# Kernel optimization log

Measured on AMD Instinct MI355X. Metric: run time of the kernel, lower is better.

Reference implementation:

```python
import jax, jax.numpy as jnp
import numpy as np

B = 1
DEPTH = 2
DIM = 256
HEADS = 8
MLP = 1024
NUM_CLASS = 4
PATCHES = 512
N = PATCHES * (NUM_CLASS + 1)  # 2560
HD = DIM // HEADS


def setup_inputs() -> dict:
    key = jax.random.key(0)
    ks = jax.random.split(key, 8)
    s = lambda k, shape: jax.random.normal(k, shape, jnp.float32) * 0.02
    return {
        "x": jax.random.normal(ks[0], (B, N, DIM), jnp.float32),
        "mask": jax.random.randint(ks[1], (B, NUM_CLASS), 0, 2, jnp.int32),
        "ln1_g": jnp.ones((DEPTH, DIM), jnp.float32),
        "ln1_b": jnp.zeros((DEPTH, DIM), jnp.float32),
        "Wqkv": s(ks[2], (DEPTH, DIM, 3 * DIM)),  # qkv_bias=False
        "Wproj": s(ks[3], (DEPTH, DIM, DIM)),
        "bproj": jnp.zeros((DEPTH, DIM), jnp.float32),
        "ln2_g": jnp.ones((DEPTH, DIM), jnp.float32),
        "ln2_b": jnp.zeros((DEPTH, DIM), jnp.float32),
        "W1": s(ks[4], (DEPTH, DIM, MLP)),
        "b1": jnp.zeros((DEPTH, MLP), jnp.float32),
        "W2": s(ks[5], (DEPTH, MLP, DIM)),
        "b2": jnp.zeros((DEPTH, DIM), jnp.float32),
    }


def layer_norm(x, g, b, eps=1e-5):
    mu = jnp.mean(x, axis=-1, keepdims=True)
    var = jnp.var(x, axis=-1, keepdims=True)
    return (x - mu) * jax.lax.rsqrt(var + eps) * g + b


def build_mask(mask):
    # Vectorized equivalent of mask_gen_fusion: block-diagonal per modality,
    # fusion rows attend everything except columns of missing modalities.
    blk = jnp.arange(N) // PATCHES  # [N], values in 0..NUM_CLASS
    base = blk[:, None] == blk[None, :]  # block diagonal (incl. fusion block)
    fusion_row = blk == NUM_CLASS  # [N]
    col_fusion = blk == NUM_CLASS  # [N]
    mod_ok = mask[:, jnp.clip(blk, 0, NUM_CLASS - 1)] == 1  # [B, N]
    allowed = jnp.where(fusion_row[None, :, None],
                        col_fusion[None, None, :] | mod_ok[:, None, :],
                        base[None, :, :])
    return allowed  # [B, N, N] bool


def reference(x, mask, ln1_g, ln1_b, Wqkv, Wproj, bproj, ln2_g, ln2_b, W1, b1, W2, b2):
    allowed = build_mask(mask)  # [B, N, N]
    scale = HD ** -0.5
    attns = []
    for d in range(DEPTH):
        # MaskedResidual(MaskedPreNormDrop(MaskedAttention))
        h = layer_norm(x, ln1_g[d], ln1_b[d])
        qkv = (h @ Wqkv[d]).reshape(B, N, 3, HEADS, HD)
        q, k, v = jnp.transpose(qkv, (2, 0, 3, 1, 4))  # each [B, H, N, HD]
        scores = jnp.einsum('bhnd,bhmd->bhnm', q, k) * scale
        scores = jnp.where(allowed[:, None, :, :], scores, -jnp.inf)
        attn = jax.nn.softmax(scores, axis=-1)  # [B, H, N, N]
        o = jnp.einsum('bhnm,bhmd->bhnd', attn, v)
        o = jnp.transpose(o, (0, 2, 1, 3)).reshape(B, N, DIM)
        o = o @ Wproj[d] + bproj[d]
        x = x + o
        attns.append(attn)
        # Residual(PreNorm(FeedForward)); F.gelu is exact erf gelu
        h2 = layer_norm(x, ln2_g[d], ln2_b[d])
        ff = jax.nn.gelu(h2 @ W1[d] + b1[d], approximate=False) @ W2[d] + b2[d]
        x = x + ff
    return x, jnp.stack(attns)
```

## Files before the change

### kernel.cpp

```cpp
#include <hip/hip_runtime.h>

#define NTOK 2560
#define NN ((long)NTOK*NTOK)

typedef __attribute__((ext_vector_type(8))) short short8;
typedef __attribute__((ext_vector_type(4))) float f32x4;

__device__ __forceinline__ unsigned short f2bf(float f){
  union { float f; unsigned int u; } v; v.f = f;
  unsigned int u = v.u + 0x7fffu + ((v.u >> 16) & 1u);
  return (unsigned short)(u >> 16);
}

__device__ __forceinline__ f32x4 mfma16(short8 a, short8 b, f32x4 c){
  return __builtin_amdgcn_mfma_f32_16x16x32_bf16(a, b, c, 0, 0, 0);
}

__global__ __launch_bounds__(256) void wt_all_k(
    const float* __restrict__ Wqkv, const float* __restrict__ Wproj,
    const float* __restrict__ W1, const float* __restrict__ W2,
    unsigned short* __restrict__ wqkvt, unsigned short* __restrict__ wprojt,
    unsigned short* __restrict__ w1t, unsigned short* __restrict__ w2t)
{
  __shared__ unsigned short T[64][68];
  int j = blockIdx.x;
  int d = j >= 192; j -= d*192;
  const float* src; unsigned short* dst; int K, N, tk, tn;
  if (j < 48){        src = Wqkv  + d*196608; dst = wqkvt  + d*196608; K=256;  N=768;  tk=j/12; tn=j-tk*12; }
  else if (j < 64){   j-=48;  src = Wproj + d*65536;  dst = wprojt + d*65536;  K=256;  N=256;  tk=j>>2; tn=j&3; }
  else if (j < 128){  j-=64;  src = W1    + d*262144; dst = w1t    + d*262144; K=256;  N=1024; tk=j>>4; tn=j&15; }
  else {              j-=128; src = W2    + d*262144; dst = w2t    + d*262144; K=1024; N=256;  tk=j>>2; tn=j&3; }
  int k0 = tk*64, n0 = tn*64;
  int r = threadIdx.x >> 2, c0 = (threadIdx.x & 3) * 16;
  const float* p = src + (long)(k0+r)*N + n0 + c0;
  #pragma unroll
  for (int e4 = 0; e4 < 4; e4++){
    f32x4 v = *(const f32x4*)(p + e4*4);
    #pragma unroll
    for (int e = 0; e < 4; e++) T[r][c0 + e4*4 + e] = f2bf(v[e]);
  }
  __syncthreads();
  unsigned short* q = dst + (long)(n0+r)*K + k0 + c0;
  short8 o0, o1;
  #pragma unroll
  for (int e = 0; e < 8; e++){ o0[e] = (short)T[c0+e][r]; o1[e] = (short)T[c0+8+e][r]; }
  *(short8*)q = o0;
  *(short8*)(q+8) = o1;
}

__device__ __forceinline__ void p_unit_body(
    int u, const unsigned short* __restrict__ qbf, const unsigned short* __restrict__ kbf,
    const float* __restrict__ rinv_ws, float* __restrict__ attn_out,
    const int* __restrict__ mask, char* smem)
{
  float (*P32)[268] = (float (*)[268])smem;
  int tid = threadIdx.x, lane = tid & 63, w = tid >> 6;
  int cb = u % 5, t2 = u / 5, tile = t2 % 80, h = t2 / 80;
  int row0 = tile * 32;
  int rblk = row0 >> 9;
  unsigned bits;
  if (rblk < 4) bits = 1u << rblk;
  else {
    bits = 16u;
    #pragma unroll
    for (int m=0; m<4; m++) if (mask[m]==1) bits |= (1u<<m);
  }
  long base = (long)h*NN + (long)row0*NTOK + cb*512;
  if (!((bits >> cb) & 1)){
    f32x4 z = {0.f,0.f,0.f,0.f};
    #pragma unroll
    for (int i=0;i<16;i++){
      int idx = tid + i*256;
      int rl = idx >> 7, c4 = (idx & 127) << 2;
      *(f32x4*)&attn_out[base + (long)rl*NTOK + c4] = z;
    }
    return;
  }
  int kk = (lane>>4)*8, l15 = lane & 15, rgrp = (lane>>4)*4;
  short8 aq0 = *(const short8*)&qbf[(h*NTOK + row0 + l15)*32 + kk];
  short8 aq1 = *(const short8*)&qbf[(h*NTOK + row0 + 16 + l15)*32 + kk];
  float rinv[8];
  #pragma unroll
  for (int r=0;r<4;r++){
    rinv[r]   = rinv_ws[h*NTOK + row0 + rgrp + r];
    rinv[4+r] = rinv_ws[h*NTOK + row0 + 16 + rgrp + r];
  }
  #pragma unroll
  for (int hf=0; hf<2; hf++){
    #pragma unroll
    for (int ct=0; ct<4; ct++){
      int cl = w*64 + ct*16 + l15;
      short8 bk = *(const short8*)&kbf[(h*NTOK + cb*512 + hf*256 + cl)*32 + kk];
      f32x4 s0 = {}; s0 = mfma16(aq0, bk, s0);
      f32x4 s1 = {}; s1 = mfma16(aq1, bk, s1);
      #pragma unroll
      for (int r=0;r<4;r++){
        P32[rgrp + r][cl]      = __expf(s0[r]) * rinv[r];
        P32[16 + rgrp + r][cl] = __expf(s1[r]) * rinv[4+r];
      }
    }
    __syncthreads();
    long hbase = base + hf*256;
    #pragma unroll
    for (int j=0;j<8;j++){
      int qi = j*256 + tid;
      int rl = qi >> 6, qc = (qi & 63)*4;
      *(f32x4*)&attn_out[hbase + (long)rl*NTOK + qc] = *(const f32x4*)&P32[rl][qc];
    }
    __syncthreads();
  }
}

template<int EPI, bool LN>
__global__ __launch_bounds__(256) void gemm2_k(
    const void* __restrict__ Ap,
    const float* __restrict__ lng, const float* __restrict__ lnb,
    const unsigned short* __restrict__ Bt,
    int N, int K,
    const float* __restrict__ bias,
    const float* __restrict__ xin,
    float* __restrict__ xout,
    unsigned short* __restrict__ obf,
    unsigned short* __restrict__ qbf,
    unsigned short* __restrict__ kbf,
    unsigned short* __restrict__ vtbf,
    int gx, int pbase,
    const unsigned short* __restrict__ p_qbf, const unsigned short* __restrict__ p_kbf,
    const float* __restrict__ p_rinv, float* __restrict__ p_attn,
    const int* __restrict__ maskp)
{
  __shared__ __align__(16) char smem[34816];
  if ((int)blockIdx.x >= gx){
    int u = pbase + ((int)blockIdx.x - gx) * (int)gridDim.y + (int)blockIdx.y;
    p_unit_body(u, p_qbf, p_kbf, p_rinv, p_attn, maskp, smem);
    return;
  }
  unsigned short (*As)[136] = (unsigned short (*)[136])smem;
  unsigned short (*Bs)[136] = (unsigned short (*)[136])(smem + 17408);
  int tid = threadIdx.x, lane = tid & 63, w = tid >> 6;
  int wr = w >> 1, wc = w & 1;
  int m0 = blockIdx.y * 64, n0 = blockIdx.x * 64;
  int row = tid >> 2, q4 = tid & 3;
  int l15 = lane & 15;
  f32x4 acc[2][2] = {};

  float mu, inv;
  if (LN){
    const float* xrow = (const float*)Ap + (m0+row)*256;
    float s = 0.f, s2 = 0.f;
    #pragma unroll
    for (int j=0;j<8;j++){
      const float* p = xrow + (j*4+q4)*8;
      f32x4 va = *(const f32x4*)p;
      f32x4 vb = *(const f32x4*)(p+4);
      #pragma unroll
      for (int e=0;e<4;e++){ s += va[e]+vb[e]; s2 += va[e]*va[e]+vb[e]*vb[e]; }
    }
    s  += __shfl_xor(s, 1);  s2 += __shfl_xor(s2, 1);
    s  += __shfl_xor(s, 2);  s2 += __shfl_xor(s2, 2);
    mu = s * (1.f/256.f);
    inv = rsqrtf(s2*(1.f/256.f) - mu*mu + 1e-5f);
  }

  for (int k0 = 0; k0 < K; k0 += 128){
    if (LN){
      const float* xrow = (const float*)Ap + (m0+row)*256;
      #pragma unroll
      for (int jj=0;jj<4;jj++){
        int cl = (jj*4+q4)*8;
        int cg = k0 + cl;
        f32x4 va = *(const f32x4*)(xrow + cg);
        f32x4 vb = *(const f32x4*)(xrow + cg + 4);
        f32x4 ga = *(const f32x4*)&lng[cg], gb = *(const f32x4*)&lng[cg+4];
        f32x4 ba = *(const f32x4*)&lnb[cg], bb = *(const f32x4*)&lnb[cg+4];
        short8 o;
        #pragma unroll
        for (int e=0;e<4;e++){
          o[e]   = (short)f2bf((va[e]-mu)*inv*ga[e] + ba[e]);
          o[4+e] = (short)f2bf((vb[e]-mu)*inv*gb[e] + bb[e]);
        }
        *(short8*)&As[row][cl] = o;
      }
    } else {
      const unsigned short* Arow = (const unsigned short*)Ap + (long)(m0+row)*K + k0;
      #pragma unroll
      for (int jj=0;jj<4;jj++){
        int cl = q4*32 + jj*8;
        *(short8*)&As[row][cl] = *(const short8*)&Arow[cl];
      }
    }
    {
      const unsigned short* Brow = Bt + (long)(n0+row)*K + k0;
      #pragma unroll
      for (int jj=0;jj<4;jj++){
        int cl = q4*32 + jj*8;
        *(short8*)&Bs[row][cl] = *(const short8*)&Brow[cl];
      }
    }
    __syncthreads();
    #pragma unroll
    for (int ks=0; ks<4; ks++){
      int kc = ks*32 + (lane>>4)*8;
      short8 a0 = *(const short8*)&As[wr*32 + l15][kc];
      short8 a1 = *(const short8*)&As[wr*32 + 16 + l15][kc];
      short8 b0 = *(const short8*)&Bs[wc*32 + l15][kc];
      short8 b1 = *(const short8*)&Bs[wc*32 + 16 + l15][kc];
      acc[0][0] = mfma16(a0,b0,acc[0][0]);
      acc[0][1] = mfma16(a0,b1,acc[0][1]);
      acc[1][0] = mfma16(a1,b0,acc[1][0]);
      acc[1][1] = mfma16(a1,b1,acc[1][1]);
    }
    if (k0 + 128 < K) __syncthreads();
  }

  #pragma unroll
  for (int rt=0; rt<2; rt++)
  #pragma unroll
  for (int ct=0; ct<2; ct++)
  #pragma unroll
  for (int r=0; r<4; r++){
    int rg = m0 + wr*32 + rt*16 + (lane>>4)*4 + r;
    int cg = n0 + wc*32 + ct*16 + l15;
    float v = acc[rt][ct][r];
    if (EPI == 0){
      int which = cg >> 8, h = (cg >> 5) & 7, hd = cg & 31;
      if (which == 0)      qbf[(h*NTOK + rg)*32 + hd] = f2bf(v * 0.17677669529663687f);
      else if (which == 1) kbf[(h*NTOK + rg)*32 + hd] = f2bf(v);
      else                 vtbf[(h*32 + hd)*NTOK + rg] = f2bf(v);
    } else if (EPI == 1){
      xout[rg*N + cg] = xin[rg*N + cg] + v + bias[cg];
    } else {
      float t = v + bias[cg];
      float ge = 0.5f * t * (1.f + erff(t * 0.70710678118654752f));
      obf[rg*N + cg] = f2bf(ge);
    }
  }
}

__global__ __launch_bounds__(256) void attn_o_k(
    const unsigned short* __restrict__ qbf,
    const unsigned short* __restrict__ kbf,
    const unsigned short* __restrict__ vtbf,
    const int* __restrict__ mask,
    float* __restrict__ rinv_ws,
    unsigned short* __restrict__ obf)
{
  __shared__ __align__(16) char asmem[34816];
  __shared__ float reds[4][32];
  __shared__ float rowinv_s[32];
  float (*P32)[268] = (float (*)[268])asmem;
  float (*O_red)[32][32] = (float (*)[32][32])asmem;

  int tid = threadIdx.x, lane = tid & 63, w = tid >> 6;
  int row0 = blockIdx.x * 32, h = blockIdx.y;
  int rblk = row0 >> 9;
  unsigned bits;
  if (rblk < 4) bits = 1u << rblk;
  else {
    bits = 16u;
    #pragma unroll
    for (int m=0; m<4; m++) if (mask[m] == 1) bits |= (1u << m);
  }
  int kk = (lane >> 4) * 8;
  int l15 = lane & 15;
  int rgrp = (lane >> 4) * 4;
  short8 aq0 = *(const short8*)&qbf[(h*NTOK + row0 + l15)*32 + kk];
  short8 aq1 = *(const short8*)&qbf[(h*NTOK + row0 + 16 + l15)*32 + kk];

  float s_[8] = {0,0,0,0,0,0,0,0};
  f32x4 oacc[2][2] = {};
  for (int b=0; b<5; b++){
    if (!((bits >> b) & 1)) continue;
    #pragma unroll
    for (int hf=0; hf<2; hf++){
      #pragma unroll
      for (int ct=0; ct<4; ct++){
        int cl = w*64 + ct*16 + l15;
        short8 bk = *(const short8*)&kbf[(h*NTOK + b*512 + hf*256 + cl)*32 + kk];
        f32x4 s0 = {}; s0 = mfma16(aq0, bk, s0);
        f32x4 s1 = {}; s1 = mfma16(aq1, bk, s1);
        #pragma unroll
        for (int r=0;r<4;r++){
          float e0 = __expf(s0[r]), e1 = __expf(s1[r]);
          s_[r] += e0; s_[4+r] += e1;
          P32[rgrp + r][cl] = e0;
          P32[16 + rgrp + r][cl] = e1;
        }
      }
      __syncthreads();
      #pragma unroll
      for (int ks2=0; ks2<2; ks2++){
        int kb = (w*2 + ks2)*32 + kk;
        f32x4 pa0a = *(const f32x4*)&P32[l15][kb],      pa0b = *(const f32x4*)&P32[l15][kb+4];
        f32x4 pa1a = *(const f32x4*)&P32[16 + l15][kb], pa1b = *(const f32x4*)&P32[16 + l15][kb+4];
        short8 pa0, pa1;
        #pragma unroll
        for (int e=0;e<4;e++){
          pa0[e] = (short)f2bf(pa0a[e]); pa0[4+e] = (short)f2bf(pa0b[e]);
          pa1[e] = (short)f2bf(pa1a[e]); pa1[4+e] = (short)f2bf(pa1b[e]);
        }
        #pragma unroll
        for (int hc=0; hc<2; hc++){
          short8 bv = *(const short8*)&vtbf[(h*32 + hc*16 + l15)*NTOK + b*512 + hf*256 + kb];
          oacc[0][hc] = mfma16(pa0, bv, oacc[0][hc]);
          oacc[1][hc] = mfma16(pa1, bv, oacc[1][hc]);
        }
      }
      __syncthreads();
    }
  }
  #pragma unroll
  for (int msk=1; msk<16; msk<<=1)
    #pragma unroll
    for (int i=0;i<8;i++) s_[i] += __shfl_xor(s_[i], msk);
  if (l15 == 0){
    #pragma unroll
    for (int r=0;r<4;r++){ reds[w][rgrp + r] = s_[r]; reds[w][16 + rgrp + r] = s_[4+r]; }
  }
  __syncthreads();
  if (tid < 32){
    float invv = 1.f / (reds[0][tid] + reds[1][tid] + reds[2][tid] + reds[3][tid]);
    rowinv_s[tid] = invv;
    rinv_ws[h*NTOK + row0 + tid] = invv;
  }
  __syncthreads();
  #pragma unroll
  for (int rt=0; rt<2; rt++)
    #pragma unroll
    for (int hc=0; hc<2; hc++)
      #pragma unroll
      for (int r=0; r<4; r++)
        O_red[w][rt*16 + rgrp + r][hc*16 + l15] = oacc[rt][hc][r];
  __syncthreads();
  #pragma unroll
  for (int i2=0; i2<2; i2++){
    int i = tid + i2*256;
    int rl = i >> 4, c2 = (i & 15) * 2;
    float invv = rowinv_s[rl];
    float o0 = (O_red[0][rl][c2]   + O_red[1][rl][c2]   + O_red[2][rl][c2]   + O_red[3][rl][c2]) * invv;
    float o1 = (O_red[0][rl][c2+1] + O_red[1][rl][c2+1] + O_red[2][rl][c2+1] + O_red[3][rl][c2+1]) * invv;
    unsigned int pk = (unsigned int)f2bf(o0) | ((unsigned int)f2bf(o1) << 16);
    *(unsigned int*)&obf[(row0 + rl)*256 + h*32 + c2] = pk;
  }
}

extern "C" void kernel_launch(void* const* d_in, const int* in_sizes, int n_in,
                              void* d_out, int out_size, void* d_ws, size_t ws_size,
                              hipStream_t stream)
{
  const float* x_in  = (const float*)d_in[0];
  const int*   maskp = (const int*)d_in[1];
  const float* ln1g  = (const float*)d_in[2];
  const float* ln1b  = (const float*)d_in[3];
  const float* Wqkv  = (const float*)d_in[4];
  const float* Wproj = (const float*)d_in[5];
  const float* bproj = (const float*)d_in[6];
  const float* ln2g  = (const float*)d_in[7];
  const float* ln2b  = (const float*)d_in[8];
  const float* W1    = (const float*)d_in[9];
  const float* b1    = (const float*)d_in[10];
  const float* W2    = (const float*)d_in[11];
  const float* b2    = (const float*)d_in[12];
  float* out = (float*)d_out;

  char* ws = (char*)d_ws;
  float* x              = (float*)(ws + 0);
  unsigned short* mbf   = (unsigned short*)(ws + 2621440);
  unsigned short* obf   = (unsigned short*)(ws + 7864320);
  unsigned short* qbf   = (unsigned short*)(ws + 9175040);
  unsigned short* kbf   = (unsigned short*)(ws + 10485760);
  unsigned short* vtbf  = (unsigned short*)(ws + 11796480);
  float* rinv           = (float*)(ws + 13107200);
  unsigned short* wqkvt = (unsigned short*)(ws + 13238272);
  unsigned short* wprojt= (unsigned short*)(ws + 14024704);
  unsigned short* w1t   = (unsigned short*)(ws + 14286848);
  unsigned short* w2t   = (unsigned short*)(ws + 15335424);

  wt_all_k<<<384, 256, 0, stream>>>(Wqkv, Wproj, W1, W2, wqkvt, wprojt, w1t, w2t);

  for (int d=0; d<2; d++){
    const float* xsrc = d ? x : x_in;
    float* attn = out + 655360 + (long)d*52428800;
    gemm2_k<0,true><<<dim3(12,40), 256, 0, stream>>>(xsrc, ln1g + d*256, ln1b + d*256,
        wqkvt + d*196608, 768, 256, nullptr, nullptr, nullptr, nullptr, qbf, kbf, vtbf,
        12, 0, nullptr, nullptr, nullptr, nullptr, nullptr);
    attn_o_k<<<dim3(80,8), 256, 0, stream>>>(qbf, kbf, vtbf, maskp, rinv, obf);
    gemm2_k<1,false><<<dim3(24,40), 256, 0, stream>>>(obf, nullptr, nullptr,
        wprojt + d*65536, 256, 256, bproj + d*256, xsrc, x, nullptr, nullptr, nullptr, nullptr,
        4, 0, qbf, kbf, rinv, attn, maskp);
    gemm2_k<2,true><<<dim3(46,40), 256, 0, stream>>>(x, ln2g + d*256, ln2b + d*256,
        w1t + d*262144, 1024, 256, b1 + d*1024, nullptr, nullptr, mbf, nullptr, nullptr, nullptr,
        16, 800, qbf, kbf, rinv, attn, maskp);
    float* xo = d ? out : x;
    gemm2_k<1,false><<<dim3(34,40), 256, 0, stream>>>(mbf, nullptr, nullptr,
        w2t + d*262144, 256, 1024, b2 + d*256, x, xo, nullptr, nullptr, nullptr, nullptr,
        4, 2000, qbf, kbf, rinv, attn, maskp);
  }
}
```

Baseline: 192.1 us.

## Fuse proj+LN2+MLP into one tail kernel and split attn zero-fill from P compute

Replaces the proj, FC1 and FC2 GEMM launches with a single tail kernel. Each 64-row block computes the projection plus residual, LayerNorm2, FC1 with GELU and FC2 on-chip, so the bf16 MLP intermediate never goes to global memory. The attention-probability output work is split into zero-fill units and real-compute units. Zero fills run alongside the QKV GEMM and the attention kernel, and the masked-in probability tiles are enumerated explicitly inside the tail kernel instead of being branch-tested per unit. This cuts launches and memory traffic, but the fused tail may have limited parallelism (40 row blocks) and heavier register use.

```diff
diff --git a/kernel.cpp b/kernel.cpp
--- a/kernel.cpp
+++ b/kernel.cpp
@@ -48,34 +48,46 @@
   *(short8*)(q+8) = o1;
 }
 
+__device__ __forceinline__ void zero_unit_body(int u, const int* __restrict__ mask,
+                                               float* __restrict__ attn_out)
+{
+  int h = u / 320, rem = u - h*320;
+  int tile, cb;
+  if (rem < 256){
+    tile = rem >> 2;
+    int zi = rem & 3, rblk = tile >> 4;
+    cb = zi + (zi >= rblk);
+  } else {
+    int fz = rem - 256;
+    tile = 64 + (fz >> 2);
+    cb = fz & 3;
+    if (mask[cb] == 1) return;
+  }
+  long base = (long)h*NN + (long)tile*32*NTOK + cb*512;
+  f32x4 z = {0.f,0.f,0.f,0.f};
+  int tid = threadIdx.x;
+  #pragma unroll
+  for (int i=0;i<16;i++){
+    int idx = tid + i*256;
+    int rl = idx >> 7, c4 = (idx & 127) << 2;
+    *(f32x4*)&attn_out[base + (long)rl*NTOK + c4] = z;
+  }
+}
+
 __device__ __forceinline__ void p_unit_body(
     int u, const unsigned short* __restrict__ qbf, const unsigned short* __restrict__ kbf,
     const float* __restrict__ rinv_ws, float* __restrict__ attn_out,
     const int* __restrict__ mask, char* smem)
 {
+  if (u >= 1152) return;
+  int h, tile, cb;
+  if (u < 512){ h = u >> 6; tile = u & 63; cb = tile >> 4; }
+  else if (u < 640){ int v = u - 512; h = v >> 4; tile = 64 + (v & 15); cb = 4; }
+  else { int v = u - 640; h = v >> 6; tile = 64 + ((v >> 2) & 15); cb = v & 3; if (mask[cb] != 1) return; }
   float (*P32)[268] = (float (*)[268])smem;
   int tid = threadIdx.x, lane = tid & 63, w = tid >> 6;
-  int cb = u % 5, t2 = u / 5, tile = t2 % 80, h = t2 / 80;
   int row0 = tile * 32;
-  int rblk = row0 >> 9;
-  unsigned bits;
-  if (rblk < 4) bits = 1u << rblk;
-  else {
-    bits = 16u;
-    #pragma unroll
-    for (int m=0; m<4; m++) if (mask[m]==1) bits |= (1u<<m);
-  }
   long base = (long)h*NN + (long)row0*NTOK + cb*512;
-  if (!((bits >> cb) & 1)){
-    f32x4 z = {0.f,0.f,0.f,0.f};
-    #pragma unroll
-    for (int i=0;i<16;i++){
-      int idx = tid + i*256;
-      int rl = idx >> 7, c4 = (idx & 127) << 2;
-      *(f32x4*)&attn_out[base + (long)rl*NTOK + c4] = z;
-    }
-    return;
-  }
   int kk = (lane>>4)*8, l15 = lane & 15, rgrp = (lane>>4)*4;
   short8 aq0 = *(const short8*)&qbf[(h*NTOK + row0 + l15)*32 + kk];
   short8 aq1 = *(const short8*)&qbf[(h*NTOK + row0 + 16 + l15)*32 + kk];
@@ -111,7 +123,7 @@
   }
 }
 
-template<int EPI, bool LN>
+template<int EPI, bool LN, int CG>
 __global__ __launch_bounds__(256) void gemm2_k(
     const void* __restrict__ Ap,
     const float* __restrict__ lng, const float* __restrict__ lnb,
@@ -124,15 +136,16 @@
     unsigned short* __restrict__ qbf,
     unsigned short* __restrict__ kbf,
     unsigned short* __restrict__ vtbf,
-    int gx, int pbase,
+    int gx, int zbase,
     const unsigned short* __restrict__ p_qbf, const unsigned short* __restrict__ p_kbf,
     const float* __restrict__ p_rinv, float* __restrict__ p_attn,
     const int* __restrict__ maskp)
 {
   __shared__ __align__(16) char smem[34816];
   if ((int)blockIdx.x >= gx){
-    int u = pbase + ((int)blockIdx.x - gx) * (int)gridDim.y + (int)blockIdx.y;
-    p_unit_body(u, p_qbf, p_kbf, p_rinv, p_attn, maskp, smem);
+    int u = zbase + ((int)blockIdx.x - gx) * (int)gridDim.y + (int)blockIdx.y;
+    if (CG == 1) zero_unit_body(u, maskp, p_attn);
+    else if (CG == 2) p_unit_body(u, p_qbf, p_kbf, p_rinv, p_attn, maskp, smem);
     return;
   }
   unsigned short (*As)[136] = (unsigned short (*)[136])smem;
@@ -229,10 +242,6 @@
       else                 vtbf[(h*32 + hd)*NTOK + rg] = f2bf(v);
     } else if (EPI == 1){
       xout[rg*N + cg] = xin[rg*N + cg] + v + bias[cg];
-    } else {
-      float t = v + bias[cg];
-      float ge = 0.5f * t * (1.f + erff(t * 0.70710678118654752f));
-      obf[rg*N + cg] = f2bf(ge);
     }
   }
 }
@@ -243,13 +252,20 @@
     const unsigned short* __restrict__ vtbf,
     const int* __restrict__ mask,
     float* __restrict__ rinv_ws,
-    unsigned short* __restrict__ obf)
+    unsigned short* __restrict__ obf,
+    int zbase, float* __restrict__ p_attn)
 {
   __shared__ __align__(16) char asmem[34816];
   __shared__ float reds[4][32];
   __shared__ float rowinv_s[32];
   float (*P32)[268] = (float (*)[268])asmem;
   float (*O_red)[32][32] = (float (*)[32][32])asmem;
+
+  if ((int)blockIdx.x >= 80){
+    int u = zbase + ((int)blockIdx.x - 80) * (int)gridDim.y + (int)blockIdx.y;
+    zero_unit_body(u, mask, p_attn);
+    return;
+  }
 
   int tid = threadIdx.x, lane = tid & 63, w = tid >> 6;
   int row0 = blockIdx.x * 32, h = blockIdx.y;
@@ -344,6 +360,169 @@
   }
 }
 
+__global__ __launch_bounds__(256, 3) void tail_k(
+    const unsigned short* __restrict__ obf,
+    const unsigned short* __restrict__ wprojt, const float* __restrict__ bproj,
+    const float* __restrict__ xin,
+    const float* __restrict__ ln2g, const float* __restrict__ ln2b,
+    const unsigned short* __restrict__ w1t, const float* __restrict__ b1,
+    const unsigned short* __restrict__ w2t, const float* __restrict__ b2,
+    float* __restrict__ xout,
+    int gx,
+    const unsigned short* __restrict__ p_qbf, const unsigned short* __restrict__ p_kbf,
+    const float* __restrict__ p_rinv, float* __restrict__ p_attn,
+    const int* __restrict__ maskp)
+{
+  __shared__ __align__(16) char smem[46080];
+  if ((int)blockIdx.x >= gx){
+    int u = ((int)blockIdx.x - gx) * (int)gridDim.y + (int)blockIdx.y;
+    p_unit_body(u, p_qbf, p_kbf, p_rinv, p_attn, maskp, smem);
+    return;
+  }
+  unsigned short (*As)[264] = (unsigned short (*)[264])smem;
+  unsigned short (*Gs)[76]  = (unsigned short (*)[76])(smem + 33792);
+  float* redS  = (float*)(smem + 43520);
+  float* redS2 = redS + 256;
+  float* muinv = redS2 + 256;
+
+  int tid = threadIdx.x, lane = tid & 63, w = tid >> 6;
+  int l15 = lane & 15, kk = (lane >> 4) * 8, rgrp = (lane >> 4) * 4;
+  int m0 = blockIdx.y * 64;
+  int cw = w * 64;
+
+  {
+    int row = tid >> 2, c0 = (tid & 3) * 64;
+    #pragma unroll
+    for (int j=0;j<8;j++)
+      *(short8*)&As[row][c0 + j*8] = *(const short8*)&obf[(m0+row)*256 + c0 + j*8];
+  }
+  __syncthreads();
+
+  f32x4 accx[4][4] = {};
+  #pragma unroll
+  for (int ks=0; ks<8; ks++){
+    int ka = ks*32 + kk;
+    short8 a[4], b[4];
+    #pragma unroll
+    for (int rt=0;rt<4;rt++) a[rt] = *(const short8*)&As[rt*16 + l15][ka];
+    #pragma unroll
+    for (int ct=0;ct<4;ct++) b[ct] = *(const short8*)&wprojt[(cw + ct*16 + l15)*256 + ka];
+    #pragma unroll
+    for (int rt=0;rt<4;rt++)
+      #pragma unroll
+      for (int ct=0;ct<4;ct++)
+        accx[rt][ct] = mfma16(a[rt], b[ct], accx[rt][ct]);
+  }
+  float rS[4][4], rS2[4][4];
+  #pragma unroll
+  for (int rt=0;rt<4;rt++)
+  #pragma unroll
+  for (int r=0;r<4;r++){
+    float s = 0.f, s2 = 0.f;
+    #pragma unroll
+    for (int ct=0;ct<4;ct++){
+      int col = cw + ct*16 + l15;
+      float v = accx[rt][ct][r] + xin[(m0 + rt*16 + rgrp + r)*256 + col] + bproj[col];
+      accx[rt][ct][r] = v;
+      s += v; s2 += v*v;
+    }
+    rS[rt][r] = s; rS2[rt][r] = s2;
+  }
+  #pragma unroll
+  for (int msk=1; msk<16; msk<<=1)
+    #pragma unroll
+    for (int rt=0;rt<4;rt++)
+      #pragma unroll
+      for (int r=0;r<4;r++){ rS[rt][r] += __shfl_xor(rS[rt][r], msk); rS2[rt][r] += __shfl_xor(rS2[rt][r], msk); }
+  if (l15 == 0){
+    #pragma unroll
+    for (int rt=0;rt<4;rt++)
+      #pragma unroll
+      for (int r=0;r<4;r++){
+        redS [w*64 + rt*16 + rgrp + r] = rS[rt][r];
+        redS2[w*64 + rt*16 + rgrp + r] = rS2[rt][r];
+      }
+  }
+  __syncthreads();
+  if (tid < 64){
+    float s  = redS[tid]  + redS[64+tid]  + redS[128+tid]  + redS[192+tid];
+    float s2 = redS2[tid] + redS2[64+tid] + redS2[128+tid] + redS2[192+tid];
+    float mu = s * (1.f/256.f);
+    float inv = rsqrtf(s2*(1.f/256.f) - mu*mu + 1e-5f);
+    muinv[tid*2] = mu; muinv[tid*2+1] = inv;
+  }
+  __syncthreads();
+  #pragma unroll
+  for (int rt=0;rt<4;rt++)
+  #pragma unroll
+  for (int ct=0;ct<4;ct++)
+  #pragma unroll
+  for (int r=0;r<4;r++){
+    int rl = rt*16 + rgrp + r;
+    int col = cw + ct*16 + l15;
+    float mu = muinv[rl*2], inv = muinv[rl*2+1];
+    float h2 = (accx[rt][ct][r] - mu)*inv*ln2g[col] + ln2b[col];
+    As[rl][col] = f2bf(h2);
+  }
+  __syncthreads();
+
+  int wr = w >> 1, wc = w & 1;
+  for (int nc=0; nc<16; nc++){
+    int n1 = nc*64;
+    f32x4 am[2][2] = {};
+    #pragma unroll
+    for (int ks=0; ks<8; ks++){
+      int ka = ks*32 + kk;
+      short8 a0 = *(const short8*)&As[wr*32 + l15][ka];
+      short8 a1 = *(const short8*)&As[wr*32 + 16 + l15][ka];
+      short8 b0 = *(const short8*)&w1t[(n1 + wc*32 + l15)*256 + ka];
+      short8 b1 = *(const short8*)&w1t[(n1 + wc*32 + 16 + l15)*256 + ka];
+      am[0][0] = mfma16(a0,b0,am[0][0]);
+      am[0][1] = mfma16(a0,b1,am[0][1]);
+      am[1][0] = mfma16(a1,b0,am[1][0]);
+      am[1][1] = mfma16(a1,b1,am[1][1]);
+    }
+    #pragma unroll
+    for (int rt2=0;rt2<2;rt2++)
+    #pragma unroll
+    for (int ct2=0;ct2<2;ct2++)
+    #pragma unroll
+    for (int r=0;r<4;r++){
+      int rl = wr*32 + rt2*16 + rgrp + r;
+      int cl = wc*32 + ct2*16 + l15;
+      float t = am[rt2][ct2][r] + b1[n1 + cl];
+      float ge = 0.5f * t * (1.f + erff(t * 0.70710678118654752f));
+      Gs[rl][cl] = f2bf(ge);
+    }
+    __syncthreads();
+    #pragma unroll
+    for (int ks2=0; ks2<2; ks2++){
+      int ka2 = ks2*32 + kk;
+      short8 a[4], b[4];
+      #pragma unroll
+      for (int rt=0;rt<4;rt++) a[rt] = *(const short8*)&Gs[rt*16 + l15][ka2];
+      #pragma unroll
+      for (int ct=0;ct<4;ct++) b[ct] = *(const short8*)&w2t[(cw + ct*16 + l15)*1024 + n1 + ka2];
+      #pragma unroll
+      for (int rt=0;rt<4;rt++)
+        #pragma unroll
+        for (int ct=0;ct<4;ct++)
+          accx[rt][ct] = mfma16(a[rt], b[ct], accx[rt][ct]);
+    }
+    __syncthreads();
+  }
+  #pragma unroll
+  for (int rt=0;rt<4;rt++)
+  #pragma unroll
+  for (int ct=0;ct<4;ct++)
+  #pragma unroll
+  for (int r=0;r<4;r++){
+    int row = m0 + rt*16 + rgrp + r;
+    int col = cw + ct*16 + l15;
+    xout[row*256 + col] = accx[rt][ct][r] + b2[col];
+  }
+}
+
 extern "C" void kernel_launch(void* const* d_in, const int* in_sizes, int n_in,
                               void* d_out, int out_size, void* d_ws, size_t ws_size,
                               hipStream_t stream)
@@ -365,35 +544,29 @@
 
   char* ws = (char*)d_ws;
   float* x              = (float*)(ws + 0);
-  unsigned short* mbf   = (unsigned short*)(ws + 2621440);
-  unsigned short* obf   = (unsigned short*)(ws + 7864320);
-  unsigned short* qbf   = (unsigned short*)(ws + 9175040);
-  unsigned short* kbf   = (unsigned short*)(ws + 10485760);
-  unsigned short* vtbf  = (unsigned short*)(ws + 11796480);
-  float* rinv           = (float*)(ws + 13107200);
-  unsigned short* wqkvt = (unsigned short*)(ws + 13238272);
-  unsigned short* wprojt= (unsigned short*)(ws + 14024704);
-  unsigned short* w1t   = (unsigned short*)(ws + 14286848);
-  unsigned short* w2t   = (unsigned short*)(ws + 15335424);
+  unsigned short* obf   = (unsigned short*)(ws + 2621440);
+  unsigned short* qbf   = (unsigned short*)(ws + 3932160);
+  unsigned short* kbf   = (unsigned short*)(ws + 5242880);
+  unsigned short* vtbf  = (unsigned short*)(ws + 6553600);
+  float* rinv           = (float*)(ws + 7864320);
+  unsigned short* wqkvt = (unsigned short*)(ws + 7995392);
+  unsigned short* wprojt= (unsigned short*)(ws + 8781824);
+  unsigned short* w1t   = (unsigned short*)(ws + 9043968);
+  unsigned short* w2t   = (unsigned short*)(ws + 10092544);
 
   wt_all_k<<<384, 256, 0, stream>>>(Wqkv, Wproj, W1, W2, wqkvt, wprojt, w1t, w2t);
 
   for (int d=0; d<2; d++){
     const float* xsrc = d ? x : x_in;
     float* attn = out + 655360 + (long)d*52428800;
-    gemm2_k<0,true><<<dim3(12,40), 256, 0, stream>>>(xsrc, ln1g + d*256, ln1b + d*256,
+    gemm2_k<0,true,1><<<dim3(32,40), 256, 0, stream>>>(xsrc, ln1g + d*256, ln1b + d*256,
         wqkvt + d*196608, 768, 256, nullptr, nullptr, nullptr, nullptr, qbf, kbf, vtbf,
-        12, 0, nullptr, nullptr, nullptr, nullptr, nullptr);
-    attn_o_k<<<dim3(80,8), 256, 0, stream>>>(qbf, kbf, vtbf, maskp, rinv, obf);
-    gemm2_k<1,false><<<dim3(24,40), 256, 0, stream>>>(obf, nullptr, nullptr,
-        wprojt + d*65536, 256, 256, bproj + d*256, xsrc, x, nullptr, nullptr, nullptr, nullptr,
-        4, 0, qbf, kbf, rinv, attn, maskp);
-    gemm2_k<2,true><<<dim3(46,40), 256, 0, stream>>>(x, ln2g + d*256, ln2b + d*256,
-        w1t + d*262144, 1024, 256, b1 + d*1024, nullptr, nullptr, mbf, nullptr, nullptr, nullptr,
-        16, 800, qbf, kbf, rinv, attn, maskp);
+        12, 0, nullptr, nullptr, nullptr, attn, maskp);
+    attn_o_k<<<dim3(300,8), 256, 0, stream>>>(qbf, kbf, vtbf, maskp, rinv, obf, 800, attn);
     float* xo = d ? out : x;
-    gemm2_k<1,false><<<dim3(34,40), 256, 0, stream>>>(mbf, nullptr, nullptr,
-        w2t + d*262144, 256, 1024, b2 + d*256, x, xo, nullptr, nullptr, nullptr, nullptr,
-        4, 2000, qbf, kbf, rinv, attn, maskp);
-  }
-}
+    tail_k<<<dim3(30,40), 256, 0, stream>>>(obf, wprojt + d*65536, bproj + d*256,
+        xsrc, ln2g + d*256, ln2b + d*256, w1t + d*262144, b1 + d*1024,
+        w2t + d*262144, b2 + d*256, xo,
+        1, qbf, kbf, rinv, attn, maskp);
+  }
+}
```

After: 390.8 us. 103% more time.
